# Kernel optimization log

Measured on AMD Instinct MI355X. Metric: run time of the kernel, lower is better.

## Reference

```python
import jax
import jax.numpy as jnp
from jax import lax
import numpy as np

B, C, Hsp, Wsp = 16, 256, 64, 64
E, HID = 4, 128          # num_experts, expert_hidden
RH = 128                 # router_hidden
TOP_K = 1
EPS = 1e-9


def setup_inputs() -> dict:
    key = jax.random.key(0)
    ks = jax.random.split(key, 8)
    s = lambda *shape: 1.0 / np.sqrt(shape[-1])
    x = jax.random.normal(ks[0], (B, C, Hsp, Wsp), dtype=jnp.float32)
    # router: Linear(C->RH), Linear(RH->E)
    Wr1 = jax.random.normal(ks[1], (RH, C), dtype=jnp.float32) * s(RH, C)
    br1 = jnp.zeros((RH,), dtype=jnp.float32)
    Wr2 = jax.random.normal(ks[2], (E, RH), dtype=jnp.float32) * s(E, RH)
    br2 = jnp.zeros((E,), dtype=jnp.float32)
    # experts (stacked over E): 1x1 C->HID, 3x3 HID->HID, 1x1 HID->C, all bias-free
    W1 = jax.random.normal(ks[3], (E, HID, C), dtype=jnp.float32) * s(E, HID, C)
    W2 = jax.random.normal(ks[4], (E, HID, HID, 3, 3), dtype=jnp.float32) * (1.0 / np.sqrt(HID * 9))
    W3 = jax.random.normal(ks[5], (E, C, HID), dtype=jnp.float32) * s(E, C, HID)
    return {"x": x, "Wr1": Wr1, "br1": br1, "Wr2": Wr2, "br2": br2,
            "W1": W1, "W2": W2, "W3": W3}


def reference(x, Wr1, br1, Wr2, br2, W1, W2, W3):
    b = x.shape[0]
    # --- router on globally pooled features ---
    pooled = x.mean(axis=(2, 3))                      # [B, C]
    h = jax.nn.relu(pooled @ Wr1.T + br1)             # [B, RH]
    logits = h @ Wr2.T + br2                          # [B, E]
    probs = jax.nn.softmax(logits, axis=1)
    # top-k masking + renormalize (top_k < num_experts)
    vals, idx = lax.top_k(probs, TOP_K)               # [B, k]
    mask = jnp.zeros_like(probs).at[jnp.arange(b)[:, None], idx].set(vals)
    probs = mask / (mask.sum(axis=1, keepdims=True) + EPS)
    # --- run all experts (as in original) ---
    # 1x1 conv C->HID, per expert:  [B, E, HID, H, W]
    y1 = jax.nn.relu(jnp.einsum('bcij,ehc->behij', x, W1))
    # 3x3 grouped conv (one group per expert), HID->HID
    y1m = y1.reshape(b, E * HID, Hsp, Wsp)
    y2 = lax.conv_general_dilated(
        y1m, W2.reshape(E * HID, HID, 3, 3),
        window_strides=(1, 1), padding='SAME',
        feature_group_count=E,
        dimension_numbers=('NCHW', 'OIHW', 'NCHW'))
    y2 = jax.nn.relu(y2).reshape(b, E, HID, Hsp, Wsp)
    # 1x1 conv HID->C fused with routed weighted sum over experts + residual
    out = jnp.einsum('begij,ecg,be->bcij', y2, W3, probs) + x
    return out
```

## Files before the change

kernel.cpp:

```cpp
#include <hip/hip_runtime.h>

typedef unsigned short ushort_t;
typedef unsigned int uint32;
typedef __attribute__((ext_vector_type(8))) short s16x8;
typedef __attribute__((ext_vector_type(4))) float f32x4;

#define BB   16
#define CC   256
#define NPX  4096
#define EE   4
#define HID  128
#define RHH  128
#define PW   66
#define PPX  (66*66)

__device__ __forceinline__ ushort_t f2bf(float f) {
  uint32 x = __float_as_uint(f);
  x += 0x7fffu + ((x >> 16) & 1u);
  return (ushort_t)(x >> 16);
}
__device__ __forceinline__ void g2l16(const void* g, void* l) {
  __builtin_amdgcn_global_load_lds((const __attribute__((address_space(1))) uint32*)g,
                                   (__attribute__((address_space(3))) uint32*)l, 16, 0, 0);
}

__global__ __launch_bounds__(256)
void k_xpose(const float* __restrict__ x, ushort_t* __restrict__ xT,
             float* __restrict__ pooled) {
  int px0 = blockIdx.x * 64, c0 = blockIdx.y * 64, b = blockIdx.z;
  int t = threadIdx.x;
  __shared__ float T[64][65];
  const float* xg = x + (size_t)b * CC * NPX;
  int cr = t >> 4, p4 = (t & 15) * 4;
#pragma unroll
  for (int i = 0; i < 4; ++i) {
    float4 v = *(const float4*)(xg + (size_t)(c0 + cr + i * 16) * NPX + px0 + p4);
    T[cr + i * 16][p4 + 0] = v.x; T[cr + i * 16][p4 + 1] = v.y;
    T[cr + i * 16][p4 + 2] = v.z; T[cr + i * 16][p4 + 3] = v.w;
  }
  __syncthreads();
  {
    int c = t >> 2, q = t & 3;
    float s = 0.f;
#pragma unroll
    for (int k = 0; k < 16; ++k) s += T[c][q * 16 + k];
    s += __shfl_down(s, 1, 64);
    s += __shfl_down(s, 2, 64);
    if (q == 0) atomicAdd(&pooled[b * CC + c0 + c], s);
  }
  int px = t >> 2, cg = (t & 3) * 16;
  uint32 o[8];
#pragma unroll
  for (int u = 0; u < 8; ++u) {
    uint32 lo = f2bf(T[cg + 2 * u][px]);
    uint32 hi = f2bf(T[cg + 2 * u + 1][px]);
    o[u] = lo | (hi << 16);
  }
  ushort_t* dst = xT + ((size_t)b * NPX + px0 + px) * CC + c0 + cg;
  *(uint4*)dst = make_uint4(o[0], o[1], o[2], o[3]);
  *(uint4*)(dst + 8) = make_uint4(o[4], o[5], o[6], o[7]);
}

__global__ __launch_bounds__(256)
void k_prep(const float* __restrict__ W1f, const float* __restrict__ W3f,
            const float* __restrict__ W2f, ushort_t* __restrict__ W1b,
            ushort_t* __restrict__ W3b, ushort_t* __restrict__ W2r) {
  int bid = blockIdx.x;
  if (bid < 256) {
    int i4 = (bid * 256 + threadIdx.x) * 4;
    const float* src; ushort_t* dst; int off;
    if (i4 < EE * HID * CC) { src = W1f; dst = W1b; off = i4; }
    else { src = W3f; dst = W3b; off = i4 - EE * HID * CC; }
    float4 v = *(const float4*)(src + off);
    ushort4 o;
    o.x = f2bf(v.x); o.y = f2bf(v.y); o.z = f2bf(v.z); o.w = f2bf(v.w);
    *(ushort4*)(dst + off) = o;
  } else {
    int i = (bid - 256) * 256 + threadIdx.x;
    int h = i & 127;
    int g = (i >> 7) & 127;
    int et = i >> 14;
    int tap = et % 9;
    int e = et / 9;
    W2r[i] = f2bf(W2f[((((size_t)e * 128 + g) * 128 + h) * 3 + tap / 3) * 3 + tap % 3]);
  }
}

__global__ __launch_bounds__(128)
void k_router(const float* __restrict__ pooled, const float* __restrict__ Wr1,
              const float* __restrict__ br1, const float* __restrict__ Wr2,
              const float* __restrict__ br2, int* __restrict__ eidx,
              float* __restrict__ gatew) {
  int b = blockIdx.x, t = threadIdx.x;
  __shared__ float hb[RHH];
  __shared__ float lg[EE];
  float s0 = 0.f;
  const float* pb = pooled + b * CC;
  const float* wr = Wr1 + t * CC;
  for (int c = 0; c < CC; ++c) s0 += pb[c] * wr[c];
  float a = br1[t] + s0 * (1.0f / NPX);
  hb[t] = a > 0.f ? a : 0.f;
  __syncthreads();
  if (t < EE) {
    float s = br2[t];
    const float* w2 = Wr2 + t * RHH;
    for (int r = 0; r < RHH; ++r) s += hb[r] * w2[r];
    lg[t] = s;
  }
  __syncthreads();
  if (t == 0) {
    float m = lg[0]; int mi = 0;
    for (int e = 1; e < EE; ++e) if (lg[e] > m) { m = lg[e]; mi = e; }
    float den = 0.f;
    for (int e = 0; e < EE; ++e) den += expf(lg[e] - m);
    float v = 1.0f / den;
    eidx[b] = mi;
    gatew[b] = v / (v + 1e-9f);
  }
}

__global__ __launch_bounds__(256)
void k_conv1(const ushort_t* __restrict__ xT, const ushort_t* __restrict__ W1b,
             const int* __restrict__ eidx, ushort_t* __restrict__ y1Tp) {
  int mt = blockIdx.x, b = blockIdx.y;
  int e = eidx[b];
  int t = threadIdx.x, wave = t >> 6, lane = t & 63;
  int wm = (wave & 1) * 64, wn = (wave >> 1) * 64;
  __shared__ ushort_t At[128 * 32];
  __shared__ ushort_t Bt[128 * 32];
  f32x4 acc[4][4] = {};
  const ushort_t* ab = xT + ((size_t)b * NPX + mt * 128) * CC;
  const ushort_t* w1 = W1b + (size_t)e * HID * CC;

  for (int ks = 0; ks < 8; ++ks) {
    int k0 = ks * 32;
    __syncthreads();
#pragma unroll
    for (int s = 0; s < 2; ++s) {
      int q = wave * 2 + s;
      int rowi = q * 16 + (lane >> 2);
      int kc = (lane & 3) * 8;
      g2l16(ab + (size_t)rowi * CC + k0 + kc, &At[q * 512]);
      g2l16(w1 + (size_t)rowi * CC + k0 + kc, &Bt[q * 512]);
    }
    __syncthreads();
    s16x8 af[4], bfr[4];
#pragma unroll
    for (int i = 0; i < 4; ++i)
      af[i] = *(const s16x8*)&At[(wm + i * 16 + (lane & 15)) * 32 + (lane >> 4) * 8];
#pragma unroll
    for (int j = 0; j < 4; ++j)
      bfr[j] = *(const s16x8*)&Bt[(wn + j * 16 + (lane & 15)) * 32 + (lane >> 4) * 8];
#pragma unroll
    for (int i = 0; i < 4; ++i)
#pragma unroll
      for (int j = 0; j < 4; ++j)
        acc[i][j] = __builtin_amdgcn_mfma_f32_16x16x32_bf16(af[i], bfr[j], acc[i][j], 0, 0, 0);
  }
  ushort_t* yb = y1Tp + (size_t)b * PPX * HID;
#pragma unroll
  for (int i = 0; i < 4; ++i) {
#pragma unroll
    for (int r = 0; r < 4; ++r) {
      int m = wm + i * 16 + (lane >> 4) * 4 + r;
      int prow = mt * 2 + (m >> 6) + 1;
      int pcol = (m & 63) + 1;
      ushort_t* row = yb + ((size_t)prow * PW + pcol) * HID + wn + (lane & 15);
#pragma unroll
      for (int j = 0; j < 4; ++j) {
        float v = acc[i][j][r];
        row[j * 16] = f2bf(v > 0.f ? v : 0.f);
      }
    }
  }
}

__global__ __launch_bounds__(256)
void k_conv2(const ushort_t* __restrict__ y1Tp, const ushort_t* __restrict__ W2r,
             const int* __restrict__ eidx, ushort_t* __restrict__ y2T) {
  int mt = blockIdx.x, b = blockIdx.y;
  int e = eidx[b];
  int t = threadIdx.x, wave = t >> 6, lane = t & 63;
  int wm = (wave & 1) * 64, wn = (wave >> 1) * 64;
  __shared__ ushort_t At[128 * 32];
  __shared__ ushort_t Bt[128 * 32];
  f32x4 acc[4][4] = {};
  const ushort_t* yb = y1Tp + (size_t)b * PPX * HID;
  const ushort_t* w2e = W2r + (size_t)e * 9 * HID * HID;

  for (int tap = 0; tap < 9; ++tap) {
    int dy = tap / 3 - 1, dx = tap % 3 - 1;
    const ushort_t* w2t = w2e + tap * HID * HID;
    for (int ks = 0; ks < 4; ++ks) {
      int k0 = ks * 32;
      __syncthreads();
#pragma unroll
      for (int s = 0; s < 2; ++s) {
        int q = wave * 2 + s;
        int rowi = q * 16 + (lane >> 2);
        int kc = (lane & 3) * 8;
        int prow = mt * 2 + (rowi >> 6) + 1 + dy;
        int pcol = (rowi & 63) + 1 + dx;
        g2l16(yb + ((size_t)prow * PW + pcol) * HID + k0 + kc, &At[q * 512]);
        g2l16(w2t + rowi * HID + k0 + kc, &Bt[q * 512]);
      }
      __syncthreads();
      s16x8 af[4], bfr[4];
#pragma unroll
      for (int i = 0; i < 4; ++i)
        af[i] = *(const s16x8*)&At[(wm + i * 16 + (lane & 15)) * 32 + (lane >> 4) * 8];
#pragma unroll
      for (int j = 0; j < 4; ++j)
        bfr[j] = *(const s16x8*)&Bt[(wn + j * 16 + (lane & 15)) * 32 + (lane >> 4) * 8];
#pragma unroll
      for (int i = 0; i < 4; ++i)
#pragma unroll
        for (int j = 0; j < 4; ++j)
          acc[i][j] = __builtin_amdgcn_mfma_f32_16x16x32_bf16(af[i], bfr[j], acc[i][j], 0, 0, 0);
    }
  }
  ushort_t* ob = y2T + ((size_t)b * NPX + (size_t)mt * 128) * HID;
#pragma unroll
  for (int i = 0; i < 4; ++i) {
#pragma unroll
    for (int r = 0; r < 4; ++r) {
      int m = wm + i * 16 + (lane >> 4) * 4 + r;
      ushort_t* row = ob + (size_t)m * HID + wn + (lane & 15);
#pragma unroll
      for (int j = 0; j < 4; ++j) {
        float v = acc[i][j][r];
        row[j * 16] = f2bf(v > 0.f ? v : 0.f);
      }
    }
  }
}

__global__ __launch_bounds__(256)
void k_conv3(const ushort_t* __restrict__ y2T, const ushort_t* __restrict__ W3b,
             const float* __restrict__ x, const int* __restrict__ eidx,
             const float* __restrict__ gatew, float* __restrict__ out) {
  int mt = blockIdx.x, nt = blockIdx.y, b = blockIdx.z;
  int e = eidx[b];
  float gw = gatew[b];
  int t = threadIdx.x, wave = t >> 6, lane = t & 63;
  int wm = (wave & 1) * 64, wn = (wave >> 1) * 64;
  __shared__ ushort_t At[128 * 32];
  __shared__ ushort_t Bt[128 * 32];
  __shared__ float Tf[32 * 132];
  f32x4 acc[4][4] = {};
  const ushort_t* yb = y2T + ((size_t)b * NPX + (size_t)mt * 128) * HID;
  const ushort_t* w3 = W3b + ((size_t)e * CC + nt * 128) * HID;

  for (int ks = 0; ks < 4; ++ks) {
    int k0 = ks * 32;
    __syncthreads();
#pragma unroll
    for (int s = 0; s < 2; ++s) {
      int q = wave * 2 + s;
      int rowi = q * 16 + (lane >> 2);
      int kc = (lane & 3) * 8;
      g2l16(yb + (size_t)rowi * HID + k0 + kc, &At[q * 512]);
      g2l16(w3 + (size_t)rowi * HID + k0 + kc, &Bt[q * 512]);
    }
    __syncthreads();
    s16x8 af[4], bfr[4];
#pragma unroll
    for (int i = 0; i < 4; ++i)
      af[i] = *(const s16x8*)&At[(wm + i * 16 + (lane & 15)) * 32 + (lane >> 4) * 8];
#pragma unroll
    for (int j = 0; j < 4; ++j)
      bfr[j] = *(const s16x8*)&Bt[(wn + j * 16 + (lane & 15)) * 32 + (lane >> 4) * 8];
#pragma unroll
    for (int i = 0; i < 4; ++i)
#pragma unroll
      for (int j = 0; j < 4; ++j)
        acc[i][j] = __builtin_amdgcn_mfma_f32_16x16x32_bf16(af[i], bfr[j], acc[i][j], 0, 0, 0);
  }
  for (int jj = 0; jj < 4; ++jj) {
    __syncthreads();
    if ((wn >> 6) == (jj >> 1)) {
      int j0 = (jj & 1) * 2;
#pragma unroll
      for (int jd = 0; jd < 2; ++jd) {
        int cl = jd * 16 + (lane & 15);
#pragma unroll
        for (int i = 0; i < 4; ++i) {
          int pb = wm + i * 16 + (lane >> 4) * 4;
          *(f32x4*)&Tf[cl * 132 + pb] = acc[i][j0 + jd];
        }
      }
    }
    __syncthreads();
#pragma unroll
    for (int it = 0; it < 4; ++it) {
      int idx = it * 256 + t;
      int crow = idx >> 5;
      int p4 = (idx & 31) * 4;
      int c = nt * 128 + jj * 32 + crow;
      int px = mt * 128 + p4;
      size_t base = ((size_t)b * CC + c) * NPX + px;
      f32x4 vv = *(const f32x4*)&Tf[crow * 132 + p4];
      f32x4 xa = *(const f32x4*)(x + base);
      vv = gw * vv + xa;
      __builtin_nontemporal_store(vv, (f32x4*)(out + base));
    }
  }
}

extern "C" void kernel_launch(void* const* d_in, const int* in_sizes, int n_in,
                              void* d_out, int out_size, void* d_ws, size_t ws_size,
                              hipStream_t stream) {
  const float* x   = (const float*)d_in[0];
  const float* Wr1 = (const float*)d_in[1];
  const float* br1 = (const float*)d_in[2];
  const float* Wr2 = (const float*)d_in[3];
  const float* br2 = (const float*)d_in[4];
  const float* W1  = (const float*)d_in[5];
  const float* W2  = (const float*)d_in[6];
  const float* W3  = (const float*)d_in[7];
  float* out = (float*)d_out;

  char* ws = (char*)d_ws;
  int*      eidx   = (int*)ws;
  float*    gatew  = (float*)(ws + 64);
  float*    pooled = (float*)(ws + 256);
  ushort_t* W1b    = (ushort_t*)(ws + 16640);
  ushort_t* W3b    = (ushort_t*)(ws + 278784);
  ushort_t* W2r    = (ushort_t*)(ws + 540928);
  ushort_t* y1Tp   = (ushort_t*)(ws + 1720576);
  ushort_t* y2T    = (ushort_t*)(ws + 19562752);
  ushort_t* xT     = (ushort_t*)d_out;

  hipMemsetAsync(y1Tp, 0, (size_t)BB * PPX * HID * 2, stream);
  hipMemsetAsync(pooled, 0, (size_t)BB * CC * 4, stream);
  k_prep  <<<2560, 256, 0, stream>>>(W1, W3, W2, W1b, W3b, W2r);
  k_xpose <<<dim3(64, 4, 16), 256, 0, stream>>>(x, xT, pooled);
  k_router<<<16, 128, 0, stream>>>(pooled, Wr1, br1, Wr2, br2, eidx, gatew);
  k_conv1 <<<dim3(32, 16), 256, 0, stream>>>(xT, W1b, eidx, y1Tp);
  k_conv2 <<<dim3(32, 16), 256, 0, stream>>>(y1Tp, W2r, eidx, y2T);
  k_conv3 <<<dim3(32, 2, 16), 256, 0, stream>>>(y2T, W3b, x, eidx, gatew, out);
}
```

Baseline: 209.5 us.

## Widen GEMM K-tile to 64 with XOR-swizzled LDS; zero only padding border

Result: faster. 195.6 us (-6.6%).

```diff
diff --git a/kernel.cpp b/kernel.cpp
--- a/kernel.cpp
+++ b/kernel.cpp
@@ -64,10 +64,11 @@
 __global__ __launch_bounds__(256)
 void k_prep(const float* __restrict__ W1f, const float* __restrict__ W3f,
             const float* __restrict__ W2f, ushort_t* __restrict__ W1b,
-            ushort_t* __restrict__ W3b, ushort_t* __restrict__ W2r) {
-  int bid = blockIdx.x;
+            ushort_t* __restrict__ W3b, ushort_t* __restrict__ W2r,
+            ushort_t* __restrict__ y1Tp, float* __restrict__ pooled) {
+  int bid = blockIdx.x, t = threadIdx.x;
   if (bid < 256) {
-    int i4 = (bid * 256 + threadIdx.x) * 4;
+    int i4 = (bid * 256 + t) * 4;
     const float* src; ushort_t* dst; int off;
     if (i4 < EE * HID * CC) { src = W1f; dst = W1b; off = i4; }
     else { src = W3f; dst = W3b; off = i4 - EE * HID * CC; }
@@ -75,14 +76,28 @@
     ushort4 o;
     o.x = f2bf(v.x); o.y = f2bf(v.y); o.z = f2bf(v.z); o.w = f2bf(v.w);
     *(ushort4*)(dst + off) = o;
-  } else {
-    int i = (bid - 256) * 256 + threadIdx.x;
+  } else if (bid < 2560) {
+    int i = (bid - 256) * 256 + t;
     int h = i & 127;
     int g = (i >> 7) & 127;
     int et = i >> 14;
     int tap = et % 9;
     int e = et / 9;
     W2r[i] = f2bf(W2f[((((size_t)e * 128 + g) * 128 + h) * 3 + tap / 3) * 3 + tap % 3]);
+  } else if (bid < 3080) {
+    int p = (bid - 2560) * 8 + (t >> 5);
+    int b = p / 260, i = p % 260;
+    int row, col;
+    if (i < 66)       { row = 0;       col = i; }
+    else if (i < 132) { row = 65;      col = i - 66; }
+    else if (i < 196) { row = i - 131; col = 0; }
+    else              { row = i - 195; col = 65; }
+    uint2* dst = (uint2*)(y1Tp + (((size_t)b * PPX + row * PW + col) * HID) + (t & 31) * 4);
+    *dst = make_uint2(0u, 0u);
+  } else {
+#pragma unroll
+    for (int i = 0; i < 4; ++i)
+      *(float4*)&pooled[t * 16 + i * 4] = make_float4(0.f, 0.f, 0.f, 0.f);
   }
 }
 
@@ -119,6 +134,36 @@
   }
 }
 
+#define STAGE64(dstA, srcA_expr, dstB, srcB_expr)                         \
+  {                                                                       \
+    _Pragma("unroll")                                                     \
+    for (int s_ = 0; s_ < 4; ++s_) {                                      \
+      int ch_ = wave * 4 + s_;                                            \
+      int r = ch_ * 8 + (lane >> 3);                                      \
+      int kc = ((lane & 7) ^ (lane >> 3)) * 8;                            \
+      g2l16(srcA_expr, &dstA[ch_ * 512]);                                 \
+      g2l16(srcB_expr, &dstB[ch_ * 512]);                                 \
+    }                                                                     \
+  }
+
+#define MFMA64(At_, Bt_)                                                  \
+  _Pragma("unroll")                                                       \
+  for (int kh = 0; kh < 2; ++kh) {                                        \
+    s16x8 af[4], bfr[4];                                                  \
+    int cidx = ((kh * 4 + (lane >> 4)) ^ (lane & 7)) * 8;                 \
+    _Pragma("unroll")                                                     \
+    for (int i = 0; i < 4; ++i)                                           \
+      af[i] = *(const s16x8*)&At_[(wm + i * 16 + (lane & 15)) * 64 + cidx]; \
+    _Pragma("unroll")                                                     \
+    for (int j = 0; j < 4; ++j)                                           \
+      bfr[j] = *(const s16x8*)&Bt_[(wn + j * 16 + (lane & 15)) * 64 + cidx]; \
+    _Pragma("unroll")                                                     \
+    for (int i = 0; i < 4; ++i)                                           \
+      _Pragma("unroll")                                                   \
+      for (int j = 0; j < 4; ++j)                                         \
+        acc[i][j] = __builtin_amdgcn_mfma_f32_16x16x32_bf16(af[i], bfr[j], acc[i][j], 0, 0, 0); \
+  }
+
 __global__ __launch_bounds__(256)
 void k_conv1(const ushort_t* __restrict__ xT, const ushort_t* __restrict__ W1b,
              const int* __restrict__ eidx, ushort_t* __restrict__ y1Tp) {
@@ -126,36 +171,19 @@
   int e = eidx[b];
   int t = threadIdx.x, wave = t >> 6, lane = t & 63;
   int wm = (wave & 1) * 64, wn = (wave >> 1) * 64;
-  __shared__ ushort_t At[128 * 32];
-  __shared__ ushort_t Bt[128 * 32];
+  __shared__ ushort_t At[128 * 64];
+  __shared__ ushort_t Bt[128 * 64];
   f32x4 acc[4][4] = {};
   const ushort_t* ab = xT + ((size_t)b * NPX + mt * 128) * CC;
   const ushort_t* w1 = W1b + (size_t)e * HID * CC;
 
-  for (int ks = 0; ks < 8; ++ks) {
-    int k0 = ks * 32;
-    __syncthreads();
-#pragma unroll
-    for (int s = 0; s < 2; ++s) {
-      int q = wave * 2 + s;
-      int rowi = q * 16 + (lane >> 2);
-      int kc = (lane & 3) * 8;
-      g2l16(ab + (size_t)rowi * CC + k0 + kc, &At[q * 512]);
-      g2l16(w1 + (size_t)rowi * CC + k0 + kc, &Bt[q * 512]);
-    }
-    __syncthreads();
-    s16x8 af[4], bfr[4];
-#pragma unroll
-    for (int i = 0; i < 4; ++i)
-      af[i] = *(const s16x8*)&At[(wm + i * 16 + (lane & 15)) * 32 + (lane >> 4) * 8];
-#pragma unroll
-    for (int j = 0; j < 4; ++j)
-      bfr[j] = *(const s16x8*)&Bt[(wn + j * 16 + (lane & 15)) * 32 + (lane >> 4) * 8];
-#pragma unroll
-    for (int i = 0; i < 4; ++i)
-#pragma unroll
-      for (int j = 0; j < 4; ++j)
-        acc[i][j] = __builtin_amdgcn_mfma_f32_16x16x32_bf16(af[i], bfr[j], acc[i][j], 0, 0, 0);
+  for (int ks = 0; ks < 4; ++ks) {
+    int k0 = ks * 64;
+    __syncthreads();
+    STAGE64(At, ab + (size_t)r * CC + k0 + kc,
+            Bt, w1 + (size_t)r * CC + k0 + kc);
+    __syncthreads();
+    MFMA64(At, Bt);
   }
   ushort_t* yb = y1Tp + (size_t)b * PPX * HID;
 #pragma unroll
@@ -182,8 +210,8 @@
   int e = eidx[b];
   int t = threadIdx.x, wave = t >> 6, lane = t & 63;
   int wm = (wave & 1) * 64, wn = (wave >> 1) * 64;
-  __shared__ ushort_t At[128 * 32];
-  __shared__ ushort_t Bt[128 * 32];
+  __shared__ ushort_t At[128 * 64];
+  __shared__ ushort_t Bt[128 * 64];
   f32x4 acc[4][4] = {};
   const ushort_t* yb = y1Tp + (size_t)b * PPX * HID;
   const ushort_t* w2e = W2r + (size_t)e * 9 * HID * HID;
@@ -191,32 +219,14 @@
   for (int tap = 0; tap < 9; ++tap) {
     int dy = tap / 3 - 1, dx = tap % 3 - 1;
     const ushort_t* w2t = w2e + tap * HID * HID;
-    for (int ks = 0; ks < 4; ++ks) {
-      int k0 = ks * 32;
+#pragma unroll
+    for (int ks = 0; ks < 2; ++ks) {
+      int k0 = ks * 64;
       __syncthreads();
-#pragma unroll
-      for (int s = 0; s < 2; ++s) {
-        int q = wave * 2 + s;
-        int rowi = q * 16 + (lane >> 2);
-        int kc = (lane & 3) * 8;
-        int prow = mt * 2 + (rowi >> 6) + 1 + dy;
-        int pcol = (rowi & 63) + 1 + dx;
-        g2l16(yb + ((size_t)prow * PW + pcol) * HID + k0 + kc, &At[q * 512]);
-        g2l16(w2t + rowi * HID + k0 + kc, &Bt[q * 512]);
-      }
+      STAGE64(At, yb + ((size_t)(mt * 2 + (r >> 6) + 1 + dy) * PW + (r & 63) + 1 + dx) * HID + k0 + kc,
+              Bt, w2t + (size_t)r * HID + k0 + kc);
       __syncthreads();
-      s16x8 af[4], bfr[4];
-#pragma unroll
-      for (int i = 0; i < 4; ++i)
-        af[i] = *(const s16x8*)&At[(wm + i * 16 + (lane & 15)) * 32 + (lane >> 4) * 8];
-#pragma unroll
-      for (int j = 0; j < 4; ++j)
-        bfr[j] = *(const s16x8*)&Bt[(wn + j * 16 + (lane & 15)) * 32 + (lane >> 4) * 8];
-#pragma unroll
-      for (int i = 0; i < 4; ++i)
-#pragma unroll
-        for (int j = 0; j < 4; ++j)
-          acc[i][j] = __builtin_amdgcn_mfma_f32_16x16x32_bf16(af[i], bfr[j], acc[i][j], 0, 0, 0);
+      MFMA64(At, Bt);
     }
   }
   ushort_t* ob = y2T + ((size_t)b * NPX + (size_t)mt * 128) * HID;
@@ -244,37 +254,21 @@
   float gw = gatew[b];
   int t = threadIdx.x, wave = t >> 6, lane = t & 63;
   int wm = (wave & 1) * 64, wn = (wave >> 1) * 64;
-  __shared__ ushort_t At[128 * 32];
-  __shared__ ushort_t Bt[128 * 32];
+  __shared__ ushort_t At[128 * 64];
+  __shared__ ushort_t Bt[128 * 64];
   __shared__ float Tf[32 * 132];
   f32x4 acc[4][4] = {};
   const ushort_t* yb = y2T + ((size_t)b * NPX + (size_t)mt * 128) * HID;
   const ushort_t* w3 = W3b + ((size_t)e * CC + nt * 128) * HID;
 
-  for (int ks = 0; ks < 4; ++ks) {
-    int k0 = ks * 32;
-    __syncthreads();
-#pragma unroll
-    for (int s = 0; s < 2; ++s) {
-      int q = wave * 2 + s;
-      int rowi = q * 16 + (lane >> 2);
-      int kc = (lane & 3) * 8;
-      g2l16(yb + (size_t)rowi * HID + k0 + kc, &At[q * 512]);
-      g2l16(w3 + (size_t)rowi * HID + k0 + kc, &Bt[q * 512]);
-    }
-    __syncthreads();
-    s16x8 af[4], bfr[4];
-#pragma unroll
-    for (int i = 0; i < 4; ++i)
-      af[i] = *(const s16x8*)&At[(wm + i * 16 + (lane & 15)) * 32 + (lane >> 4) * 8];
-#pragma unroll
-    for (int j = 0; j < 4; ++j)
-      bfr[j] = *(const s16x8*)&Bt[(wn + j * 16 + (lane & 15)) * 32 + (lane >> 4) * 8];
-#pragma unroll
-    for (int i = 0; i < 4; ++i)
-#pragma unroll
-      for (int j = 0; j < 4; ++j)
-        acc[i][j] = __builtin_amdgcn_mfma_f32_16x16x32_bf16(af[i], bfr[j], acc[i][j], 0, 0, 0);
+#pragma unroll
+  for (int ks = 0; ks < 2; ++ks) {
+    int k0 = ks * 64;
+    __syncthreads();
+    STAGE64(At, yb + (size_t)r * HID + k0 + kc,
+            Bt, w3 + (size_t)r * HID + k0 + kc);
+    __syncthreads();
+    MFMA64(At, Bt);
   }
   for (int jj = 0; jj < 4; ++jj) {
     __syncthreads();
@@ -331,9 +325,7 @@
   ushort_t* y2T    = (ushort_t*)(ws + 19562752);
   ushort_t* xT     = (ushort_t*)d_out;
 
-  hipMemsetAsync(y1Tp, 0, (size_t)BB * PPX * HID * 2, stream);
-  hipMemsetAsync(pooled, 0, (size_t)BB * CC * 4, stream);
-  k_prep  <<<2560, 256, 0, stream>>>(W1, W3, W2, W1b, W3b, W2r);
+  k_prep  <<<3081, 256, 0, stream>>>(W1, W3, W2, W1b, W3b, W2r, y1Tp, pooled);
   k_xpose <<<dim3(64, 4, 16), 256, 0, stream>>>(x, xT, pooled);
   k_router<<<16, 128, 0, stream>>>(pooled, Wr1, br1, Wr2, br2, eidx, gatew);
   k_conv1 <<<dim3(32, 16), 256, 0, stream>>>(xT, W1b, eidx, y1Tp);
```
